# Performance work log

Measured on AMD Instinct MI355X. Metric: run time of the kernel, lower is better.

The kernel has to match this reference:

```python
import jax, jax.numpy as jnp
import numpy as np

B, S, IK, IV = 16, 2048, 3, 1
D = IK + IV          # input_size = 4
H = 256              # hidden_size
F = 512              # dim_feedforward
L = 2                # num_layers
EPS = 1e-5


def setup_inputs() -> dict:
    key = jax.random.key(0)
    ks = jax.random.split(key, 16)
    n = jax.random.normal
    inp = {
        'KEY': n(ks[0], (B, S, IK), jnp.float32),
        'VALUE': n(ks[1], (B, S, IV), jnp.float32),
        # per-layer kernel-attention projections (stacked on layer axis)
        'Wq': n(ks[2], (L, D, H), jnp.float32) * 0.1,
        'bq': jnp.zeros((L, H), jnp.float32),
        'Wk': n(ks[3], (L, D, H), jnp.float32) * 0.1,
        'bk': jnp.zeros((L, H), jnp.float32),
        'Wv': n(ks[4], (L, D, H), jnp.float32) * 0.1,
        'bv': jnp.zeros((L, H), jnp.float32),
        'Wo': n(ks[5], (L, H, D), jnp.float32) * 0.1,
        'bo': jnp.zeros((L, D), jnp.float32),
        'bw': jnp.ones((L,), jnp.float32),          # Gaussian kernel bandwidth
        # LayerNorm 1
        'g1': jnp.ones((L, D), jnp.float32),
        'be1': jnp.zeros((L, D), jnp.float32),
        # FFN
        'W1': n(ks[6], (L, D, F), jnp.float32) * 0.1,
        'b1': jnp.zeros((L, F), jnp.float32),
        'W2': n(ks[7], (L, F, D), jnp.float32) * 0.1,
        'b2': jnp.zeros((L, D), jnp.float32),
        # LayerNorm 2
        'g2': jnp.ones((L, D), jnp.float32),
        'be2': jnp.zeros((L, D), jnp.float32),
        # final fc: input_size -> input_v
        'Wfc': n(ks[8], (D, IV), jnp.float32) * 0.1,
        'bfc': jnp.zeros((IV,), jnp.float32),
    }
    return inp


def _layernorm(x, g, b):
    m = x.mean(-1, keepdims=True)
    v = ((x - m) ** 2).mean(-1, keepdims=True)
    return (x - m) * jax.lax.rsqrt(v + EPS) * g + b


def reference(KEY, VALUE, Wq, bq, Wk, bk, Wv, bv, Wo, bo, bw,
              g1, be1, W1, b1, W2, b2, g2, be2, Wfc, bfc):
    # positioning: concat coords and values -> [B, S, D]
    X = jnp.concatenate([KEY, VALUE], axis=-1)
    n_layers = Wq.shape[0]
    for i in range(n_layers):
        # Nadaraya-Watson Gaussian kernel attention (madsnn, type='nwd', kernel='gauss')
        Q = X @ Wq[i] + bq[i]                      # [B,S,H]
        K = X @ Wk[i] + bk[i]                      # [B,S,H]
        V = X @ Wv[i] + bv[i]                      # [B,S,H]
        # pairwise squared distances ||q-k||^2, [B,S,S]
        d2 = ((Q * Q).sum(-1)[:, :, None]
              + (K * K).sum(-1)[:, None, :]
              - 2.0 * jnp.einsum('bqh,bkh->bqk', Q, K))
        attn = jax.nn.softmax(-0.5 * d2 * (bw[i] ** 2), axis=-1)
        attn_out = jnp.einsum('bqk,bkh->bqh', attn, V) @ Wo[i] + bo[i]  # [B,S,D]
        # residual + LayerNorm + FFN + residual + LayerNorm (dropout = identity in eval)
        res = _layernorm(X + attn_out, g1[i], be1[i])
        ff = jax.nn.relu(res @ W1[i] + b1[i]) @ W2[i] + b2[i]
        X = _layernorm(res + ff, g2[i], be2[i])
    return X @ Wfc + bfc                            # [B,S,IV]
```

## Files before the change

kernel.cpp:

```cpp
#include <hip/hip_runtime.h>

#define BB 16
#define SS 2048
#define NTOK (BB*SS)
#define FF 512
#define EPSF 1e-5f

#if __has_builtin(__builtin_amdgcn_exp2f)
#define EXP2F(x) __builtin_amdgcn_exp2f(x)
#else
#define EXP2F(x) exp2f(x)
#endif

typedef float v2f __attribute__((ext_vector_type(2)));


__device__ __forceinline__ float wred64(float v) {
#pragma unroll
  for (int m = 32; m > 0; m >>= 1) v += __shfl_xor(v, m, 64);
  return v;
}


__global__ __launch_bounds__(256) void prep_kernel(
    const float* __restrict__ KEY, const float* __restrict__ VALUE,
    const float* __restrict__ Wq, const float* __restrict__ bq,
    const float* __restrict__ Wk, const float* __restrict__ bk,
    const float* __restrict__ Wv, const float* __restrict__ bv,
    const float* __restrict__ Wo, const float* __restrict__ bw,
    const float* __restrict__ W1, const float* __restrict__ b1,
    const float* __restrict__ W2,
    float* __restrict__ sm, float* __restrict__ w1t, float* __restrict__ X0)
{
  const int bid = blockIdx.x;
  if (bid < 128) {
    const int gq = bid*256 + threadIdx.x;
    *(float4*)(X0 + (size_t)gq*4) =
        make_float4(KEY[gq*3 + 0], KEY[gq*3 + 1], KEY[gq*3 + 2], VALUE[gq]);
    return;
  }
  const int i = bid - 128;
  if (threadIdx.x >= 64) return;
  const int lane = threadIdx.x;
  float m4[4][4] = {{0}}, gkk[4][4] = {{0}}, wvo[4][4] = {{0}};
  float akk[4] = {0}, bvo[4] = {0};
  float ck1 = 0.f, ck2 = 0.f;

  for (int h = lane; h < 256; h += 64) {
    float vq[4], vk[4], vv[4], wo4[4];
#pragma unroll
    for (int a = 0; a < 4; ++a) {
      vq[a]  = Wq[(i*4 + a)*256 + h];
      vk[a]  = Wk[(i*4 + a)*256 + h];
      vv[a]  = Wv[(i*4 + a)*256 + h];
      wo4[a] = Wo[(i*256 + h)*4 + a];
    }
    const float bqh = bq[i*256 + h], bkh = bk[i*256 + h], bvh = bv[i*256 + h];
#pragma unroll
    for (int a = 0; a < 4; ++a) {
#pragma unroll
      for (int c = 0; c < 4; ++c) {
        m4[a][c]  = fmaf(vq[a], vk[c], m4[a][c]);
        gkk[a][c] = fmaf(vk[a], vk[c], gkk[a][c]);
        wvo[a][c] = fmaf(vv[a], wo4[c], wvo[a][c]);
      }
      akk[a] = fmaf(vk[a], bqh - bkh, akk[a]);
      bvo[a] = fmaf(bvh, wo4[a], bvo[a]);
    }
    ck1 = fmaf(bqh, bkh, ck1);
    ck2 = fmaf(bkh, bkh, ck2);
  }
#pragma unroll
  for (int a = 0; a < 4; ++a) {
#pragma unroll
    for (int c = 0; c < 4; ++c) {
      m4[a][c]  = wred64(m4[a][c]);
      gkk[a][c] = wred64(gkk[a][c]);
      wvo[a][c] = wred64(wvo[a][c]);
    }
    akk[a] = wred64(akk[a]);
    bvo[a] = wred64(bvo[a]);
  }
  ck1 = wred64(ck1); ck2 = wred64(ck2);

  if (lane == 0) {
    const float bwv = bw[i];
    const float bw2 = bwv * bwv * 1.44269504088896f;
    float* s = sm + i*64;
#pragma unroll
    for (int a = 0; a < 4; ++a) {
#pragma unroll
      for (int c = 0; c < 4; ++c) {
        s[a*4+c]      = bw2 * m4[a][c];
        s[16 + a*4+c] = -0.5f * bw2 * gkk[a][c];
        s[32 + a*4+c] = wvo[a][c];
      }
      s[48+a] = bw2 * akk[a];
      s[52+a] = bvo[a];
    }
    s[56] = bw2 * (ck1 - 0.5f * ck2);
  }
  for (int f = lane; f < FF; f += 64) {
    float* rec = w1t + (i*FF + f)*12;
#pragma unroll
    for (int c = 0; c < 4; ++c) rec[c]   = W1[(i*4 + c)*FF + f];
#pragma unroll
    for (int c = 0; c < 4; ++c) rec[4+c] = W2[(i*FF + f)*4 + c];
    rec[8] = b1[i*FF + f];
    rec[9] = 0.f; rec[10] = 0.f; rec[11] = 0.f;
  }
}

__device__ __forceinline__ void compute_feat(const float x[4], const float* __restrict__ s,
                                             float* __restrict__ featrec)
{
  float P[4], VT[4], tk[4];
#pragma unroll
  for (int a = 0; a < 4; ++a) {
    P[a]  = fmaf(s[a*4+3], x[3], fmaf(s[a*4+2], x[2], fmaf(s[a*4+1], x[1], s[a*4+0]*x[0])));
    tk[a] = fmaf(s[16+a*4+3], x[3], fmaf(s[16+a*4+2], x[2], fmaf(s[16+a*4+1], x[1], s[16+a*4+0]*x[0])));
    VT[a] = s[52+a] + fmaf(s[32+3*4+a], x[3], fmaf(s[32+2*4+a], x[2], fmaf(s[32+1*4+a], x[1], s[32+0*4+a]*x[0])));
  }
  float R = s[56];
#pragma unroll
  for (int a = 0; a < 4; ++a) R = fmaf(tk[a] + s[48+a], x[a], R);
  float4* fp = (float4*)featrec;
  fp[0] = make_float4(P[0], P[1], P[2], P[3]);
  fp[1] = make_float4(VT[0], VT[1], VT[2], VT[3]);
  fp[2] = make_float4(R, 0.f, 0.f, 0.f);
}

__global__ __launch_bounds__(256) void attn_kernel(
    const float* __restrict__ X, const float* __restrict__ sm,
    float* __restrict__ part)
{
  __shared__ float smem[512*21];
  const int bid = blockIdx.x;
  const int b = bid >> 5;
  const int r = bid & 31;
  const int qg = r >> 3, kb = r & 7;
  const int qbase = (b << 11) + (qg << 9);
  const int kbase = (b << 11) + (kb << 8);
  const int tid = threadIdx.x;
  const int lane = tid & 63, wave = tid >> 6;

  {
    const float4 xk = *(const float4*)(X + (size_t)(kbase + tid)*4);
    float xr[4] = {xk.x, xk.y, xk.z, xk.w};
    float fr[12];
    compute_feat(xr, sm, fr);
    float* dst = smem + tid*12;
    ((float4*)dst)[0] = ((float4*)fr)[0];
    ((float4*)dst)[1] = ((float4*)fr)[1];
    dst[8] = fr[8];
  }

  v2f xq2[4][4], axy[8], azw[8], ad[4];
#pragma unroll
  for (int jp = 0; jp < 4; ++jp) {
    const float4 xa = *(const float4*)(X + (size_t)(qbase + (2*jp  )*64 + lane)*4);
    const float4 xb = *(const float4*)(X + (size_t)(qbase + (2*jp+1)*64 + lane)*4);
    xq2[jp][0] = v2f{xa.x, xb.x};
    xq2[jp][1] = v2f{xa.y, xb.y};
    xq2[jp][2] = v2f{xa.z, xb.z};
    xq2[jp][3] = v2f{xa.w, xb.w};
    ad[jp] = v2f{0.f, 0.f};
  }
#pragma unroll
  for (int j = 0; j < 8; ++j) { axy[j] = v2f{0.f, 0.f}; azw[j] = v2f{0.f, 0.f}; }
  __syncthreads();

  const float* kf = smem + wave*64*12;
#pragma unroll 2
  for (int k = 0; k < 64; ++k) {
    const float* kp = kf + k*12;
    const float4 P  = *(const float4*)kp;
    const float4 VT = *(const float4*)(kp + 4);
    const float R = kp[8];
    const v2f Rv  = v2f{R, R};
    const v2f Px  = v2f{P.x, P.x}, Py = v2f{P.y, P.y};
    const v2f Pz  = v2f{P.z, P.z}, Pw = v2f{P.w, P.w};
    const v2f Vxy = v2f{VT.x, VT.y}, Vzw = v2f{VT.z, VT.w};
#pragma unroll
    for (int jp = 0; jp < 4; ++jp) {
      v2f l = __builtin_elementwise_fma(xq2[jp][0], Px, Rv);
      l = __builtin_elementwise_fma(xq2[jp][1], Py, l);
      l = __builtin_elementwise_fma(xq2[jp][2], Pz, l);
      l = __builtin_elementwise_fma(xq2[jp][3], Pw, l);
      const float e0 = EXP2F(l.x);
      const float e1 = EXP2F(l.y);
      const v2f e0v = v2f{e0, e0}, e1v = v2f{e1, e1};
      axy[2*jp  ] = __builtin_elementwise_fma(e0v, Vxy, axy[2*jp  ]);
      azw[2*jp  ] = __builtin_elementwise_fma(e0v, Vzw, azw[2*jp  ]);
      axy[2*jp+1] = __builtin_elementwise_fma(e1v, Vxy, axy[2*jp+1]);
      azw[2*jp+1] = __builtin_elementwise_fma(e1v, Vzw, azw[2*jp+1]);
      ad[jp] += v2f{e0, e1};
    }
  }
  __syncthreads();
#pragma unroll
  for (int j = 0; j < 8; ++j) {
    float* rr = smem + (j*64 + lane)*21 + wave*5;
    rr[0] = axy[j].x; rr[1] = axy[j].y; rr[2] = azw[j].x;
    rr[3] = azw[j].y; rr[4] = (j & 1) ? ad[j>>1].y : ad[j>>1].x;
  }
  __syncthreads();
  float* pb = part + (size_t)kb * NTOK * 8;
#pragma unroll
  for (int t = 0; t < 2; ++t) {
    const int q = t*256 + tid;
    const float* rr = smem + q*21;
    float s0 = 0.f, s1 = 0.f, s2 = 0.f, s3 = 0.f, s4 = 0.f;
#pragma unroll
    for (int w = 0; w < 4; ++w) {
      s0 += rr[w*5+0]; s1 += rr[w*5+1]; s2 += rr[w*5+2];
      s3 += rr[w*5+3]; s4 += rr[w*5+4];
    }
    float* pp = pb + (size_t)(qbase + q)*8;
    *(float4*)pp = make_float4(s0, s1, s2, s3);
    pp[4] = s4;
  }
}

__device__ __forceinline__ void ln4(const float t[4], const float* __restrict__ g,
                                    const float* __restrict__ b, float r[4])
{
  const float m = 0.25f*(t[0]+t[1]+t[2]+t[3]);
  const float d0 = t[0]-m, d1 = t[1]-m, d2 = t[2]-m, d3 = t[3]-m;
  const float v = 0.25f*(d0*d0 + d1*d1 + d2*d2 + d3*d3);
  const float sc = rsqrtf(v + EPSF);
  r[0] = fmaf(d0*sc, g[0], b[0]);
  r[1] = fmaf(d1*sc, g[1], b[1]);
  r[2] = fmaf(d2*sc, g[2], b[2]);
  r[3] = fmaf(d3*sc, g[3], b[3]);
}

__global__ __launch_bounds__(512) void combine_kernel(
    const float* __restrict__ part, const float* __restrict__ Xin,
    const float* __restrict__ w1t,
    const float* __restrict__ bo, const float* __restrict__ g1, const float* __restrict__ be1,
    const float* __restrict__ b2v, const float* __restrict__ g2, const float* __restrict__ be2,
    float* __restrict__ Xout,
    const float* __restrict__ Wfc, const float* __restrict__ bfc,
    float* __restrict__ outp, int last)
{
  const int tok = threadIdx.x & 63, fc = threadIdx.x >> 6;
  const int gq = blockIdx.x*64 + tok;
  __shared__ float redp[8][64][5];
  __shared__ float ress[64][4];
  __shared__ float redf[8][64][4];

  {
    const float* pp = part + ((size_t)fc*NTOK + gq)*8;
    const float4 v = *(const float4*)pp;
    redp[fc][tok][0] = v.x; redp[fc][tok][1] = v.y;
    redp[fc][tok][2] = v.z; redp[fc][tok][3] = v.w;
    redp[fc][tok][4] = pp[4];
  }
  __syncthreads();

  if (fc == 0) {
    float acc[5] = {0,0,0,0,0};
#pragma unroll
    for (int k = 0; k < 8; ++k)
#pragma unroll
      for (int c = 0; c < 5; ++c) acc[c] += redp[k][tok][c];
    const float inv = 1.0f / acc[4];
    const float4 xv = *(const float4*)(Xin + (size_t)gq*4);
    float t[4];
    t[0] = xv.x + fmaf(acc[0], inv, bo[0]);
    t[1] = xv.y + fmaf(acc[1], inv, bo[1]);
    t[2] = xv.z + fmaf(acc[2], inv, bo[2]);
    t[3] = xv.w + fmaf(acc[3], inv, bo[3]);
    float r[4];
    ln4(t, g1, be1, r);
    ress[tok][0] = r[0]; ress[tok][1] = r[1]; ress[tok][2] = r[2]; ress[tok][3] = r[3];
  }
  __syncthreads();

  const float r0 = ress[tok][0], r1 = ress[tok][1], r2 = ress[tok][2], r3 = ress[tok][3];
  float fa[4] = {0,0,0,0};
  const float* wt = w1t + (size_t)fc*64*12;
#pragma unroll 4
  for (int f = 0; f < 64; ++f) {
    const float* rec = wt + f*12;
    const float4 w1r = *(const float4*)rec;
    const float4 w2r = *(const float4*)(rec + 4);
    const float b1f = rec[8];
    float h = fmaf(r3, w1r.w, fmaf(r2, w1r.z, fmaf(r1, w1r.y, fmaf(r0, w1r.x, b1f))));
    h = fmaxf(h, 0.f);
    fa[0] = fmaf(h, w2r.x, fa[0]);
    fa[1] = fmaf(h, w2r.y, fa[1]);
    fa[2] = fmaf(h, w2r.z, fa[2]);
    fa[3] = fmaf(h, w2r.w, fa[3]);
  }
  redf[fc][tok][0] = fa[0]; redf[fc][tok][1] = fa[1];
  redf[fc][tok][2] = fa[2]; redf[fc][tok][3] = fa[3];
  __syncthreads();

  if (fc == 0) {
    float t2[4];
#pragma unroll
    for (int c = 0; c < 4; ++c) {
      float s = b2v[c];
#pragma unroll
      for (int k = 0; k < 8; ++k) s += redf[k][tok][c];
      t2[c] = ress[tok][c] + s;
    }
    float y[4];
    ln4(t2, g2, be2, y);
    if (last) {
      outp[gq] = fmaf(y[3], Wfc[3], fmaf(y[2], Wfc[2], fmaf(y[1], Wfc[1], fmaf(y[0], Wfc[0], bfc[0]))));
    } else {
      *(float4*)(Xout + (size_t)gq*4) = make_float4(y[0], y[1], y[2], y[3]);
    }
  }
}

extern "C" void kernel_launch(void* const* d_in, const int* in_sizes, int n_in,
                              void* d_out, int out_size, void* d_ws, size_t ws_size,
                              hipStream_t stream)
{
  const float* KEY   = (const float*)d_in[0];
  const float* VALUE = (const float*)d_in[1];
  const float* Wq  = (const float*)d_in[2];
  const float* bq  = (const float*)d_in[3];
  const float* Wk  = (const float*)d_in[4];
  const float* bk  = (const float*)d_in[5];
  const float* Wv  = (const float*)d_in[6];
  const float* bv  = (const float*)d_in[7];
  const float* Wo  = (const float*)d_in[8];
  const float* bo  = (const float*)d_in[9];
  const float* bw  = (const float*)d_in[10];
  const float* g1  = (const float*)d_in[11];
  const float* be1 = (const float*)d_in[12];
  const float* W1  = (const float*)d_in[13];
  const float* b1  = (const float*)d_in[14];
  const float* W2  = (const float*)d_in[15];
  const float* b2  = (const float*)d_in[16];
  const float* g2  = (const float*)d_in[17];
  const float* be2 = (const float*)d_in[18];
  const float* Wfc = (const float*)d_in[19];
  const float* bfc = (const float*)d_in[20];
  float* out = (float*)d_out;

  float* w    = (float*)d_ws;
  float* sm   = w;
  float* w1t  = w + 128;
  float* X0   = w + 12416;
  float* X1   = w + 143488;
  float* part = w + 274560;

  prep_kernel<<<130, 256, 0, stream>>>(KEY, VALUE, Wq, bq, Wk, bk, Wv, bv, Wo, bw,
                                       W1, b1, W2, sm, w1t, X0);

  attn_kernel<<<512, 256, 0, stream>>>(X0, sm, part);
  combine_kernel<<<512, 512, 0, stream>>>(part, X0, w1t,
      bo, g1, be1, b2, g2, be2,
      X1, Wfc, bfc, out, 0);

  attn_kernel<<<512, 256, 0, stream>>>(X1, sm + 64, part);
  combine_kernel<<<512, 512, 0, stream>>>(part, X1, w1t + FF*12,
      bo + 4, g1 + 4, be1 + 4, b2 + 4, g2 + 4, be2 + 4,
      X0, Wfc, bfc, out, 1);
}
```

Before: 183.5 us.

## Fuse attention with combine/FFN per query tile and precompute key features

Merges the separate attention and combine kernels into one layer kernel. Each block covers 64 queries against all 2048 keys, reduces the partial sums across waves in shared memory, then runs LayerNorm, FFN and the next LayerNorm in place. Key features are computed once per layer, in a small kernel or in the previous layer's epilogue, and read from global memory. This removes the per-key-block partial-sum buffer round trip and the repeated feature computation in every block. The cost is that each key load now serves only 2 queries per lane instead of 8, so the inner loop does more global/L1 loads per exp.

```diff
diff --git a/kernel.cpp b/kernel.cpp
--- a/kernel.cpp
+++ b/kernel.cpp
@@ -130,96 +130,18 @@
   fp[2] = make_float4(R, 0.f, 0.f, 0.f);
 }
 
-__global__ __launch_bounds__(256) void attn_kernel(
-    const float* __restrict__ X, const float* __restrict__ sm,
-    float* __restrict__ part)
-{
-  __shared__ float smem[512*21];
-  const int bid = blockIdx.x;
-  const int b = bid >> 5;
-  const int r = bid & 31;
-  const int qg = r >> 3, kb = r & 7;
-  const int qbase = (b << 11) + (qg << 9);
-  const int kbase = (b << 11) + (kb << 8);
-  const int tid = threadIdx.x;
-  const int lane = tid & 63, wave = tid >> 6;
-
-  {
-    const float4 xk = *(const float4*)(X + (size_t)(kbase + tid)*4);
-    float xr[4] = {xk.x, xk.y, xk.z, xk.w};
-    float fr[12];
-    compute_feat(xr, sm, fr);
-    float* dst = smem + tid*12;
-    ((float4*)dst)[0] = ((float4*)fr)[0];
-    ((float4*)dst)[1] = ((float4*)fr)[1];
-    dst[8] = fr[8];
-  }
-
-  v2f xq2[4][4], axy[8], azw[8], ad[4];
-#pragma unroll
-  for (int jp = 0; jp < 4; ++jp) {
-    const float4 xa = *(const float4*)(X + (size_t)(qbase + (2*jp  )*64 + lane)*4);
-    const float4 xb = *(const float4*)(X + (size_t)(qbase + (2*jp+1)*64 + lane)*4);
-    xq2[jp][0] = v2f{xa.x, xb.x};
-    xq2[jp][1] = v2f{xa.y, xb.y};
-    xq2[jp][2] = v2f{xa.z, xb.z};
-    xq2[jp][3] = v2f{xa.w, xb.w};
-    ad[jp] = v2f{0.f, 0.f};
-  }
-#pragma unroll
-  for (int j = 0; j < 8; ++j) { axy[j] = v2f{0.f, 0.f}; azw[j] = v2f{0.f, 0.f}; }
-  __syncthreads();
-
-  const float* kf = smem + wave*64*12;
-#pragma unroll 2
-  for (int k = 0; k < 64; ++k) {
-    const float* kp = kf + k*12;
-    const float4 P  = *(const float4*)kp;
-    const float4 VT = *(const float4*)(kp + 4);
-    const float R = kp[8];
-    const v2f Rv  = v2f{R, R};
-    const v2f Px  = v2f{P.x, P.x}, Py = v2f{P.y, P.y};
-    const v2f Pz  = v2f{P.z, P.z}, Pw = v2f{P.w, P.w};
-    const v2f Vxy = v2f{VT.x, VT.y}, Vzw = v2f{VT.z, VT.w};
-#pragma unroll
-    for (int jp = 0; jp < 4; ++jp) {
-      v2f l = __builtin_elementwise_fma(xq2[jp][0], Px, Rv);
-      l = __builtin_elementwise_fma(xq2[jp][1], Py, l);
-      l = __builtin_elementwise_fma(xq2[jp][2], Pz, l);
-      l = __builtin_elementwise_fma(xq2[jp][3], Pw, l);
-      const float e0 = EXP2F(l.x);
-      const float e1 = EXP2F(l.y);
-      const v2f e0v = v2f{e0, e0}, e1v = v2f{e1, e1};
-      axy[2*jp  ] = __builtin_elementwise_fma(e0v, Vxy, axy[2*jp  ]);
-      azw[2*jp  ] = __builtin_elementwise_fma(e0v, Vzw, azw[2*jp  ]);
-      axy[2*jp+1] = __builtin_elementwise_fma(e1v, Vxy, axy[2*jp+1]);
-      azw[2*jp+1] = __builtin_elementwise_fma(e1v, Vzw, azw[2*jp+1]);
-      ad[jp] += v2f{e0, e1};
-    }
-  }
-  __syncthreads();
-#pragma unroll
-  for (int j = 0; j < 8; ++j) {
-    float* rr = smem + (j*64 + lane)*21 + wave*5;
-    rr[0] = axy[j].x; rr[1] = axy[j].y; rr[2] = azw[j].x;
-    rr[3] = azw[j].y; rr[4] = (j & 1) ? ad[j>>1].y : ad[j>>1].x;
-  }
-  __syncthreads();
-  float* pb = part + (size_t)kb * NTOK * 8;
-#pragma unroll
-  for (int t = 0; t < 2; ++t) {
-    const int q = t*256 + tid;
-    const float* rr = smem + q*21;
-    float s0 = 0.f, s1 = 0.f, s2 = 0.f, s3 = 0.f, s4 = 0.f;
-#pragma unroll
-    for (int w = 0; w < 4; ++w) {
-      s0 += rr[w*5+0]; s1 += rr[w*5+1]; s2 += rr[w*5+2];
-      s3 += rr[w*5+3]; s4 += rr[w*5+4];
-    }
-    float* pp = pb + (size_t)(qbase + q)*8;
-    *(float4*)pp = make_float4(s0, s1, s2, s3);
-    pp[4] = s4;
-  }
+__global__ __launch_bounds__(256) void feat_kernel(
+    const float* __restrict__ X, const float* __restrict__ sm, float* __restrict__ feat)
+{
+  const int gq = blockIdx.x*256 + threadIdx.x;
+  const float4 xv = *(const float4*)(X + (size_t)gq*4);
+  float xr[4] = {xv.x, xv.y, xv.z, xv.w};
+  float fr[12];
+  compute_feat(xr, sm, fr);
+  float4* fp = (float4*)(feat + (size_t)gq*12);
+  fp[0] = ((float4*)fr)[0];
+  fp[1] = ((float4*)fr)[1];
+  fp[2] = ((float4*)fr)[2];
 }
 
 __device__ __forceinline__ void ln4(const float t[4], const float* __restrict__ g,
@@ -235,51 +157,95 @@
   r[3] = fmaf(d3*sc, g[3], b[3]);
 }
 
-__global__ __launch_bounds__(512) void combine_kernel(
-    const float* __restrict__ part, const float* __restrict__ Xin,
-    const float* __restrict__ w1t,
+__global__ __launch_bounds__(512, 4) void layer_kernel(
+    const float* __restrict__ X, const float* __restrict__ feat,
+    const float* __restrict__ w1t, const float* __restrict__ smn,
     const float* __restrict__ bo, const float* __restrict__ g1, const float* __restrict__ be1,
     const float* __restrict__ b2v, const float* __restrict__ g2, const float* __restrict__ be2,
-    float* __restrict__ Xout,
+    float* __restrict__ Xout, float* __restrict__ featout,
     const float* __restrict__ Wfc, const float* __restrict__ bfc,
     float* __restrict__ outp, int last)
 {
-  const int tok = threadIdx.x & 63, fc = threadIdx.x >> 6;
-  const int gq = blockIdx.x*64 + tok;
-  __shared__ float redp[8][64][5];
+  const int bid = blockIdx.x;
+  const int b = bid >> 5, qg = bid & 31;
+  const int qbase = (b << 11) + (qg << 6);
+  const int tid = threadIdx.x;
+  const int lane = tid & 63, wave = tid >> 6;
+  const int j = lane & 31, half = lane >> 5;
+
+  __shared__ float red[8][32][12];
   __shared__ float ress[64][4];
   __shared__ float redf[8][64][4];
 
+  v2f xq0, xq1, xq2v, xq3;
   {
-    const float* pp = part + ((size_t)fc*NTOK + gq)*8;
-    const float4 v = *(const float4*)pp;
-    redp[fc][tok][0] = v.x; redp[fc][tok][1] = v.y;
-    redp[fc][tok][2] = v.z; redp[fc][tok][3] = v.w;
-    redp[fc][tok][4] = pp[4];
+    const float4 xa = *(const float4*)(X + (size_t)(qbase + 2*j    )*4);
+    const float4 xb = *(const float4*)(X + (size_t)(qbase + 2*j + 1)*4);
+    xq0  = v2f{xa.x, xb.x}; xq1 = v2f{xa.y, xb.y};
+    xq2v = v2f{xa.z, xb.z}; xq3 = v2f{xa.w, xb.w};
+  }
+  v2f a0xy = v2f{0.f,0.f}, a0zw = v2f{0.f,0.f};
+  v2f a1xy = v2f{0.f,0.f}, a1zw = v2f{0.f,0.f};
+  v2f ad   = v2f{0.f,0.f};
+
+  const float* kp = feat + (size_t)((b << 11) + (wave*2 + half)*128) * 12;
+#pragma unroll 4
+  for (int k = 0; k < 128; ++k) {
+    const float4 P  = *(const float4*)(kp + k*12);
+    const float4 VT = *(const float4*)(kp + k*12 + 4);
+    const float  R  = kp[k*12 + 8];
+    v2f l = __builtin_elementwise_fma(xq0, v2f{P.x, P.x}, v2f{R, R});
+    l = __builtin_elementwise_fma(xq1,  v2f{P.y, P.y}, l);
+    l = __builtin_elementwise_fma(xq2v, v2f{P.z, P.z}, l);
+    l = __builtin_elementwise_fma(xq3,  v2f{P.w, P.w}, l);
+    const float e0 = EXP2F(l.x);
+    const float e1 = EXP2F(l.y);
+    const v2f Vxy = v2f{VT.x, VT.y}, Vzw = v2f{VT.z, VT.w};
+    const v2f e0v = v2f{e0, e0}, e1v = v2f{e1, e1};
+    a0xy = __builtin_elementwise_fma(e0v, Vxy, a0xy);
+    a0zw = __builtin_elementwise_fma(e0v, Vzw, a0zw);
+    a1xy = __builtin_elementwise_fma(e1v, Vxy, a1xy);
+    a1zw = __builtin_elementwise_fma(e1v, Vzw, a1zw);
+    ad += v2f{e0, e1};
+  }
+
+  float v10[10] = {a0xy.x, a0xy.y, a0zw.x, a0zw.y,
+                   a1xy.x, a1xy.y, a1zw.x, a1zw.y, ad.x, ad.y};
+#pragma unroll
+  for (int c = 0; c < 10; ++c) v10[c] += __shfl_xor(v10[c], 32, 64);
+  if (half == 0) {
+    float* rr = &red[wave][j][0];
+    *(float4*)rr       = make_float4(v10[0], v10[1], v10[2], v10[3]);
+    *(float4*)(rr + 4) = make_float4(v10[4], v10[5], v10[6], v10[7]);
+    rr[8] = v10[8]; rr[9] = v10[9];
   }
   __syncthreads();
 
-  if (fc == 0) {
-    float acc[5] = {0,0,0,0,0};
-#pragma unroll
-    for (int k = 0; k < 8; ++k)
-#pragma unroll
-      for (int c = 0; c < 5; ++c) acc[c] += redp[k][tok][c];
-    const float inv = 1.0f / acc[4];
-    const float4 xv = *(const float4*)(Xin + (size_t)gq*4);
-    float t[4];
-    t[0] = xv.x + fmaf(acc[0], inv, bo[0]);
-    t[1] = xv.y + fmaf(acc[1], inv, bo[1]);
-    t[2] = xv.z + fmaf(acc[2], inv, bo[2]);
-    t[3] = xv.w + fmaf(acc[3], inv, bo[3]);
+  if (tid < 64) {
+    const int jj = tid >> 1, p = tid & 1;
+    float sv0 = 0.f, sv1 = 0.f, sv2 = 0.f, sv3 = 0.f, sd = 0.f;
+#pragma unroll
+    for (int w = 0; w < 8; ++w) {
+      const float4 vv = *(const float4*)&red[w][jj][p*4];
+      sv0 += vv.x; sv1 += vv.y; sv2 += vv.z; sv3 += vv.w;
+      sd  += red[w][jj][8 + p];
+    }
+    const float inv = 1.0f / sd;
+    const float4 xv = *(const float4*)(X + (size_t)(qbase + tid)*4);
+    float t4[4];
+    t4[0] = xv.x + fmaf(sv0, inv, bo[0]);
+    t4[1] = xv.y + fmaf(sv1, inv, bo[1]);
+    t4[2] = xv.z + fmaf(sv2, inv, bo[2]);
+    t4[3] = xv.w + fmaf(sv3, inv, bo[3]);
     float r[4];
-    ln4(t, g1, be1, r);
-    ress[tok][0] = r[0]; ress[tok][1] = r[1]; ress[tok][2] = r[2]; ress[tok][3] = r[3];
+    ln4(t4, g1, be1, r);
+    *(float4*)&ress[tid][0] = make_float4(r[0], r[1], r[2], r[3]);
   }
   __syncthreads();
 
-  const float r0 = ress[tok][0], r1 = ress[tok][1], r2 = ress[tok][2], r3 = ress[tok][3];
-  float fa[4] = {0,0,0,0};
+  const int tok = lane, fc = wave;
+  const float4 rv = *(const float4*)&ress[tok][0];
+  float fa0 = 0.f, fa1 = 0.f, fa2 = 0.f, fa3 = 0.f;
   const float* wt = w1t + (size_t)fc*64*12;
 #pragma unroll 4
   for (int f = 0; f < 64; ++f) {
@@ -287,32 +253,38 @@
     const float4 w1r = *(const float4*)rec;
     const float4 w2r = *(const float4*)(rec + 4);
     const float b1f = rec[8];
-    float h = fmaf(r3, w1r.w, fmaf(r2, w1r.z, fmaf(r1, w1r.y, fmaf(r0, w1r.x, b1f))));
+    float h = fmaf(rv.w, w1r.w, fmaf(rv.z, w1r.z, fmaf(rv.y, w1r.y, fmaf(rv.x, w1r.x, b1f))));
     h = fmaxf(h, 0.f);
-    fa[0] = fmaf(h, w2r.x, fa[0]);
-    fa[1] = fmaf(h, w2r.y, fa[1]);
-    fa[2] = fmaf(h, w2r.z, fa[2]);
-    fa[3] = fmaf(h, w2r.w, fa[3]);
-  }
-  redf[fc][tok][0] = fa[0]; redf[fc][tok][1] = fa[1];
-  redf[fc][tok][2] = fa[2]; redf[fc][tok][3] = fa[3];
+    fa0 = fmaf(h, w2r.x, fa0);
+    fa1 = fmaf(h, w2r.y, fa1);
+    fa2 = fmaf(h, w2r.z, fa2);
+    fa3 = fmaf(h, w2r.w, fa3);
+  }
+  *(float4*)&redf[fc][tok][0] = make_float4(fa0, fa1, fa2, fa3);
   __syncthreads();
 
-  if (fc == 0) {
+  if (tid < 64) {
     float t2[4];
 #pragma unroll
     for (int c = 0; c < 4; ++c) {
       float s = b2v[c];
 #pragma unroll
-      for (int k = 0; k < 8; ++k) s += redf[k][tok][c];
-      t2[c] = ress[tok][c] + s;
+      for (int k = 0; k < 8; ++k) s += redf[k][tid][c];
+      t2[c] = ress[tid][c] + s;
     }
     float y[4];
     ln4(t2, g2, be2, y);
+    const int gq = qbase + tid;
     if (last) {
       outp[gq] = fmaf(y[3], Wfc[3], fmaf(y[2], Wfc[2], fmaf(y[1], Wfc[1], fmaf(y[0], Wfc[0], bfc[0]))));
     } else {
       *(float4*)(Xout + (size_t)gq*4) = make_float4(y[0], y[1], y[2], y[3]);
+      float fr[12];
+      compute_feat(y, smn, fr);
+      float4* fp = (float4*)(featout + (size_t)gq*12);
+      fp[0] = ((float4*)fr)[0];
+      fp[1] = ((float4*)fr)[1];
+      fp[2] = ((float4*)fr)[2];
     }
   }
 }
@@ -349,18 +321,18 @@
   float* w1t  = w + 128;
   float* X0   = w + 12416;
   float* X1   = w + 143488;
-  float* part = w + 274560;
+  float* f0   = w + 274560;
+  float* f1   = w + 667776;
 
   prep_kernel<<<130, 256, 0, stream>>>(KEY, VALUE, Wq, bq, Wk, bk, Wv, bv, Wo, bw,
                                        W1, b1, W2, sm, w1t, X0);
-
-  attn_kernel<<<512, 256, 0, stream>>>(X0, sm, part);
-  combine_kernel<<<512, 512, 0, stream>>>(part, X0, w1t,
+  feat_kernel<<<128, 256, 0, stream>>>(X0, sm, f0);
+
+  layer_kernel<<<512, 512, 0, stream>>>(X0, f0, w1t, sm + 64,
       bo, g1, be1, b2, g2, be2,
-      X1, Wfc, bfc, out, 0);
-
-  attn_kernel<<<512, 256, 0, stream>>>(X1, sm + 64, part);
-  combine_kernel<<<512, 512, 0, stream>>>(part, X1, w1t + FF*12,
+      X1, f1, Wfc, bfc, out, 0);
+
+  layer_kernel<<<512, 512, 0, stream>>>(X1, f1, w1t + FF*12, sm,
       bo + 4, g1 + 4, be1 + 4, b2 + 4, g2 + 4, be2 + 4,
-      X0, Wfc, bfc, out, 1);
-}
+      X0, f0, Wfc, bfc, out, 1);
+}
```

New measurement: 210.6 us. 1.15x slower.
